# Kernel tuning notes

Measured on AMD Instinct MI355X. Metric: run time of the kernel, lower is better.

Reference implementation:

```python
import jax, jax.numpy as jnp
import numpy as np

B, C, IC, H, W = 16, 256, 128, 32, 32  # batch, in_channels, inter_channels, spatial
EPS = 1e-5


def _conv1x1(x, w, b=None):
    # x: [B,C,H,W], w: [O,C] -> [B,O,H,W]
    y = jnp.einsum('bchw,oc->bohw', x, w)
    if b is not None:
        y = y + b[None, :, None, None]
    return y


def _dot_kernel(x, wt, wp):
    # relu-matmul attention, symmetrized, degree-rsqrt normalized with zero masking
    b, _, h, w = x.shape
    n = h * w
    t = jnp.maximum(_conv1x1(x, wt), 0.0).reshape(b, -1, n)  # [B,IC,N]
    p = jnp.maximum(_conv1x1(x, wp), 0.0).reshape(b, -1, n)  # [B,IC,N]
    att = jnp.einsum('bcn,bcm->bnm', t, p)                    # [B,N,N]
    att = (att + att.transpose(0, 2, 1)) * 0.5
    d = att.sum(axis=2)                                       # [B,N]
    dinv = jnp.where(d != 0, jax.lax.rsqrt(jnp.where(d != 0, d, 1.0)), 0.0)
    return att * dinv[:, None, :] * dinv[:, :, None]


def _bn(x, gamma, beta):
    # BatchNorm2d in training mode (batch statistics, biased variance)
    mu = jnp.mean(x, axis=(0, 2, 3), keepdims=True)
    var = jnp.mean((x - mu) ** 2, axis=(0, 2, 3), keepdims=True)
    xhat = (x - mu) * jax.lax.rsqrt(var + EPS)
    return xhat * gamma[None, :, None, None] + beta[None, :, None, None]


def setup_inputs() -> dict:
    key = jax.random.key(0)
    ks = jax.random.split(key, 32)
    s = 0.05
    inp = {
        'x':  jax.random.normal(ks[0], (B, C, H, W), jnp.float32),
        'ob': jax.random.normal(ks[1], (B, C, H, W), jnp.float32),
        'od': jax.random.normal(ks[2], (B, C, H, W), jnp.float32),
        'Wt': jax.random.normal(ks[3], (IC, C), jnp.float32) * s,
        'Wp': jax.random.normal(ks[4], (IC, C), jnp.float32) * s,
        'Wgx': jax.random.normal(ks[5], (IC, C), jnp.float32) * s,
        'bgx': jax.random.normal(ks[6], (IC,), jnp.float32) * s,
        'Wgb': jax.random.normal(ks[7], (IC, C), jnp.float32) * s,
        'bgb': jax.random.normal(ks[8], (IC,), jnp.float32) * s,
        'Wgd': jax.random.normal(ks[9], (IC, C), jnp.float32) * s,
        'bgd': jax.random.normal(ks[10], (IC,), jnp.float32) * s,
        'Wwx': jax.random.normal(ks[11], (C, IC), jnp.float32) * s,
        'bwx': jax.random.normal(ks[12], (C,), jnp.float32) * s,
        'Wwb': jax.random.normal(ks[13], (C, IC), jnp.float32) * s,
        'bwb': jax.random.normal(ks[14], (C,), jnp.float32) * s,
        'Wwd': jax.random.normal(ks[15], (C, IC), jnp.float32) * s,
        'bwd': jax.random.normal(ks[16], (C,), jnp.float32) * s,
        'Wwxb': jax.random.normal(ks[17], (C, IC), jnp.float32) * s,
        'bwxb': jax.random.normal(ks[18], (C,), jnp.float32) * s,
        'Wwxd': jax.random.normal(ks[19], (C, IC), jnp.float32) * s,
        'bwxd': jax.random.normal(ks[20], (C,), jnp.float32) * s,
        'gamma1': jnp.ones((C,), jnp.float32),
        'beta1': jnp.zeros((C,), jnp.float32),
        'gamma2': jnp.ones((C,), jnp.float32),
        'beta2': jnp.zeros((C,), jnp.float32),
        'Wout': jax.random.normal(ks[21], (C, C), jnp.float32) * s,
        'bout': jax.random.normal(ks[22], (C,), jnp.float32) * s,
    }
    return inp


def reference(x, ob, od, Wt, Wp, Wgx, bgx, Wgb, bgb, Wgd, bgd,
              Wwx, bwx, Wwb, bwb, Wwd, bwd, Wwxb, bwxb, Wwxd, bwxd,
              gamma1, beta1, gamma2, beta2, Wout, bout):
    b, c, h, w = x.shape
    n = h * w

    def g_tokens(inp, wg, bg):
        return _conv1x1(inp, wg, bg).reshape(b, -1, n).transpose(0, 2, 1)  # [B,N,IC]

    g_x = g_tokens(x, Wgx, bgx)
    g_b = g_tokens(ob, Wgb, bgb)
    g_d = g_tokens(od, Wgd, bgd)

    f_x = _dot_kernel(x, Wt, Wp)
    f_b = _dot_kernel(ob, Wt, Wp)
    f_d = _dot_kernel(od, Wt, Wp)

    def agg(f, g):
        # bmm(f,g).transpose(1,2).view(B,IC,H,W)
        return jnp.einsum('bnm,bmi->bin', f, g).reshape(b, -1, h, w)

    x_self = _conv1x1(agg(f_x, g_x), Wwx, bwx)
    ob_self = _conv1x1(agg(f_b, g_b), Wwb, bwb)
    od_self = _conv1x1(agg(f_d, g_d), Wwd, bwd)
    x_ob_cross = _conv1x1(agg(f_b, g_x), Wwxb, bwxb)
    x_od_cross = _conv1x1(agg(f_d, g_x), Wwxd, bwxd)

    od_final = _bn(od_self + x_ob_cross, gamma1, beta1)
    ob_final = _bn(ob_self + x_od_cross, gamma2, beta2)
    output = _conv1x1(od_final + ob_final + x_self, Wout, bout)
    return output + x
```

## Files before the change

kernel.cpp:

```cpp
#include <hip/hip_runtime.h>

#define GAS __attribute__((address_space(1)))
#define LAS __attribute__((address_space(3)))

typedef __attribute__((ext_vector_type(8))) short short8;
typedef __attribute__((ext_vector_type(4))) float f32x4;
typedef unsigned short u16;

constexpr int cB = 16, cC = 256, cIC = 128, cN = 1024;

__device__ __forceinline__ u16 f2bf(float v) {
    unsigned u = __builtin_bit_cast(unsigned, v);
    return (u16)((u + 0x7fffu + ((u >> 16) & 1u)) >> 16);
}
__device__ __forceinline__ float bf2f(u16 v) {
    unsigned u = ((unsigned)v) << 16;
    return __builtin_bit_cast(float, u);
}
__device__ __forceinline__ float rsz(float d) {
    return (d != 0.0f) ? rsqrtf(d) : 0.0f;
}

template<int N> __device__ __forceinline__ void wait_vmcnt() {
    if constexpr (N == 0) asm volatile("s_waitcnt vmcnt(0)" ::: "memory");
    else if constexpr (N == 1) asm volatile("s_waitcnt vmcnt(1)" ::: "memory");
    else if constexpr (N == 2) asm volatile("s_waitcnt vmcnt(2)" ::: "memory");
    else if constexpr (N == 3) asm volatile("s_waitcnt vmcnt(3)" ::: "memory");
    else if constexpr (N == 4) asm volatile("s_waitcnt vmcnt(4)" ::: "memory");
    else if constexpr (N == 5) asm volatile("s_waitcnt vmcnt(5)" ::: "memory");
    else if constexpr (N == 6) asm volatile("s_waitcnt vmcnt(6)" ::: "memory");
}

template<int BM, int BN, int WR, int WC, bool BREMAP = false>
__device__ __forceinline__ void gemm_core(
    const u16* __restrict__ Ab, const u16* __restrict__ Ab2, int ksplit, int lda,
    const u16* __restrict__ Bb, int ldb, int K,
    u16* lsA, u16* lsB,
    f32x4 (&acc)[BM/(WR*16)][BN/(WC*16)])
{
    constexpr int THREADS = WR * WC * 64;
    constexpr int MR = BM / (WR * 16), NR = BN / (WC * 16);
    constexpr int ACH = (BM * 64) / (THREADS * 16);
    constexpr int BCH = (BN * 64) / (THREADS * 16);
    constexpr int RPC = THREADS / 4;
    constexpr int ISSUES = ACH + BCH;

    const int tid  = threadIdx.x;
    const int lane = tid & 63;
    const int wave = tid >> 6;
    const int wr = wave / WC, wc = wave % WC;
    const int r0 = tid >> 2, slot = tid & 3;

    auto stage = [&](int buf, int kk) {
        const u16* Ak = (Ab2 != nullptr && kk >= ksplit) ? (Ab2 + (kk - ksplit)) : (Ab + kk);
        const u16* Bk = Bb + (BREMAP ? (((kk >> 7) << 8) + (kk & 127)) : kk);
        #pragma unroll
        for (int c = 0; c < ACH; c++) {
            int row = c * RPC + r0;
            int sk = (slot ^ ((row >> 1) & 3)) << 3;
            __builtin_amdgcn_global_load_lds((GAS void*)(Ak + (size_t)row * lda + sk),
                (LAS void*)(lsA + buf * (BM * 32) + c * (THREADS * 8) + (wave << 9)), 16, 0, 0);
        }
        #pragma unroll
        for (int c = 0; c < BCH; c++) {
            int row = c * RPC + r0;
            int sk = (slot ^ ((row >> 1) & 3)) << 3;
            __builtin_amdgcn_global_load_lds((GAS void*)(Bk + (size_t)row * ldb + sk),
                (LAS void*)(lsB + buf * (BN * 32) + c * (THREADS * 8) + (wave << 9)), 16, 0, 0);
        }
    };

    stage(0, 0);
    const int nt = K >> 5;
    for (int t = 0; t < nt; t++) {
        const int cur = t & 1;
        if (t + 1 < nt) { stage(cur ^ 1, (t + 1) << 5); wait_vmcnt<ISSUES>(); }
        else            wait_vmcnt<0>();
        __builtin_amdgcn_s_barrier();
        asm volatile("" ::: "memory");

        const u16* la = lsA + cur * (BM * 32);
        const u16* lb = lsB + cur * (BN * 32);
        short8 af[MR], bf[NR];
        #pragma unroll
        for (int m = 0; m < MR; m++) {
            int row = wr * (BM / WR) + (m << 4) + (lane & 15);
            af[m] = *(const short8*)&la[(row << 5) + (((lane >> 4) ^ ((row >> 1) & 3)) << 3)];
        }
        #pragma unroll
        for (int n = 0; n < NR; n++) {
            int row = wc * (BN / WC) + (n << 4) + (lane & 15);
            bf[n] = *(const short8*)&lb[(row << 5) + (((lane >> 4) ^ ((row >> 1) & 3)) << 3)];
        }
        #pragma unroll
        for (int m = 0; m < MR; m++)
            #pragma unroll
            for (int n = 0; n < NR; n++)
                acc[m][n] = __builtin_amdgcn_mfma_f32_16x16x32_bf16(af[m], bf[n], acc[m][n], 0, 0, 0);

        asm volatile("s_waitcnt lgkmcnt(0)" ::: "memory");
        __builtin_amdgcn_sched_barrier(0);
        __builtin_amdgcn_s_barrier();
    }
}

template<int BM, int BN, int WR, int WC, bool RELU, bool OBF16, bool RBIAS, bool RESID>
__global__ __launch_bounds__(WR*WC*64) void gemm_bt(
    const u16* __restrict__ A, long long sA, long long sA2, int lda,
    const u16* __restrict__ B, long long sB, long long sB2, int ldb,
    void* __restrict__ C, long long sC, long long sC2, int ldc,
    int K,
    const float* __restrict__ bias, int sb2,
    const float* __restrict__ resid, long long sR)
{
    __shared__ alignas(16) u16 lsA[2 * BM * 32];
    __shared__ alignas(16) u16 lsB[2 * BN * 32];

    const int lane = threadIdx.x & 63;
    const int wave = threadIdx.x >> 6;
    const int wr = wave / WC, wc = wave % WC;
    const int zlo = blockIdx.z & 15, zhi = blockIdx.z >> 4;

    const u16* Ab = A + zlo * sA + zhi * sA2 + (size_t)(blockIdx.x * BM) * lda;
    const u16* Bb = B + zlo * sB + zhi * sB2 + (size_t)(blockIdx.y * BN) * ldb;

    f32x4 acc[BM/(WR*16)][BN/(WC*16)] = {};
    gemm_core<BM, BN, WR, WC>(Ab, nullptr, K, lda, Bb, ldb, K, lsA, lsB, acc);

    const int rowb = blockIdx.x * BM + wr * (BM / WR) + ((lane >> 4) << 2);
    const int colb = blockIdx.y * BN + wc * (BN / WC) + (lane & 15);
    const long long cbase = zlo * sC + zhi * sC2;
    #pragma unroll
    for (int m = 0; m < BM/(WR*16); m++) {
        #pragma unroll
        for (int n = 0; n < BN/(WC*16); n++) {
            #pragma unroll
            for (int r = 0; r < 4; r++) {
                int row = rowb + m * 16 + r;
                int col = colb + n * 16;
                float v = acc[m][n][r];
                if (RBIAS) v += bias[zhi * sb2 + row];
                if (RESID) v += resid[zlo * sR + (size_t)row * ldc + col];
                if (RELU)  v = fmaxf(v, 0.0f);
                if (OBF16) ((u16*)C)[cbase + (size_t)row * ldc + col] = f2bf(v);
                else       ((float*)C)[cbase + (size_t)row * ldc + col] = v;
            }
        }
    }
}

__global__ __launch_bounds__(512) void tp_gemm(
    const u16* __restrict__ XT, const u16* __restrict__ WTP,
    u16* __restrict__ TPt, u16* __restrict__ TP, float* __restrict__ CS)
{
    __shared__ alignas(16) u16 lsA[2 * 128 * 32];
    __shared__ alignas(16) u16 lsB[2 * 256 * 32];

    const int id = blockIdx.x;
    const int lane = threadIdx.x & 63;
    const int wave = threadIdx.x >> 6;
    const int wr = wave >> 2, wc = wave & 3;

    if (id < 384) {
        const int z = id >> 3, r_ = id & 7, cx = r_ >> 2, ny = r_ & 3;
        const u16* Ab = WTP + (size_t)(cx * 128) * 256;
        const u16* Bb = XT + (size_t)z * 262144 + (size_t)(ny * 256) * 256;
        f32x4 acc[4][4] = {};
        gemm_core<128, 256, 2, 4>(Ab, nullptr, 256, 256, Bb, 256, 256, lsA, lsB, acc);

        const int rowb = cx * 128 + wr * 64 + ((lane >> 4) << 2);
        const int colb = ny * 256 + wc * 64 + (lane & 15);
        u16* Cb = TPt + (size_t)z * 262144;
        float rp[4][4] = {};
        #pragma unroll
        for (int m = 0; m < 4; m++)
            #pragma unroll
            for (int n = 0; n < 4; n++)
                #pragma unroll
                for (int r = 0; r < 4; r++) {
                    float v = fmaxf(acc[m][n][r], 0.0f);
                    Cb[(size_t)(rowb + m * 16 + r) * 1024 + colb + n * 16] = f2bf(v);
                    rp[m][r] += v;
                }
        #pragma unroll
        for (int m = 0; m < 4; m++)
            #pragma unroll
            for (int r = 0; r < 4; r++) {
                float v = rp[m][r];
                v += __shfl_xor(v, 1, 64);
                v += __shfl_xor(v, 2, 64);
                v += __shfl_xor(v, 4, 64);
                v += __shfl_xor(v, 8, 64);
                if ((lane & 15) == 0)
                    atomicAdd(&CS[z * 256 + rowb + m * 16 + r], v);
            }
    } else {
        const int id2 = id - 384;
        const int z = id2 >> 3, nx = id2 & 7;
        const u16* Ab = XT + (size_t)z * 262144 + (size_t)(nx * 128) * 256;
        f32x4 acc[4][4] = {};
        gemm_core<128, 256, 2, 4>(Ab, nullptr, 256, 256, WTP, 256, 256, lsA, lsB, acc);

        const int rowb = nx * 128 + wr * 64 + ((lane >> 4) << 2);
        const int colb = wc * 64 + (lane & 15);
        u16* Cb = TP + (size_t)z * 262144;
        #pragma unroll
        for (int m = 0; m < 4; m++)
            #pragma unroll
            for (int n = 0; n < 4; n++)
                #pragma unroll
                for (int r = 0; r < 4; r++)
                    Cb[(size_t)(rowb + m * 16 + r) * 256 + colb + n * 16] =
                        f2bf(fmaxf(acc[m][n][r], 0.0f));
    }
}

__global__ __launch_bounds__(256) void dinv_mv(
    const u16* __restrict__ TPt, const float* __restrict__ CS, float* __restrict__ DINV)
{
    const int z = blockIdx.y;
    const int n = blockIdx.x * 256 + threadIdx.x;
    __shared__ float ws[256];
    ws[threadIdx.x] = 0.5f * CS[z * 256 + (threadIdx.x ^ 128)];
    __syncthreads();
    const u16* base = TPt + (size_t)z * 262144 + n;
    float d = 0;
    #pragma unroll 8
    for (int c = 0; c < 256; c++) d += bf2f(base[(size_t)c << 10]) * ws[c];
    DINV[(z << 10) + n] = d;
}

__global__ __launch_bounds__(256) void g_gemm(
    const u16* __restrict__ XT, const u16* __restrict__ WG,
    const float* __restrict__ BG, const float* __restrict__ DINV,
    u16* __restrict__ GXp, u16* __restrict__ GBp, u16* __restrict__ GDp)
{
    __shared__ alignas(16) u16 lsA[2 * 128 * 32];
    __shared__ alignas(16) u16 lsB[2 * 128 * 32];

    const int yb = blockIdx.x, zs = blockIdx.z;
    const int stream = zs >> 4, b = zs & 15;

    const u16* Ab = WG + stream * 32768;
    const u16* Bb = XT + (size_t)zs * 262144 + (size_t)(yb * 128) * 256;

    f32x4 acc[4][4] = {};
    gemm_core<128, 128, 2, 2>(Ab, nullptr, 256, 256, Bb, 256, 256, lsA, lsB, acc);

    const int lane = threadIdx.x & 63;
    const int wave = threadIdx.x >> 6;
    const int wr = wave >> 1, wc = wave & 1;
    const int rowb = (wr << 6) + ((lane >> 4) << 2);
    const int colb = yb * 128 + (wc << 6) + (lane & 15);
    const float* dvx = DINV + (b << 10);
    const float* dvb = DINV + 16384 + (b << 10);
    const float* dvd = DINV + 32768 + (b << 10);
    float sx[4], sb_[4], sd[4];
    #pragma unroll
    for (int n = 0; n < 4; n++) {
        int col = colb + n * 16;
        if (stream == 0) { sx[n] = rsz(dvx[col]); sb_[n] = rsz(dvb[col]); sd[n] = rsz(dvd[col]); }
        else if (stream == 1) sb_[n] = rsz(dvb[col]);
        else sd[n] = rsz(dvd[col]);
    }
    #pragma unroll
    for (int m = 0; m < 4; m++) {
        #pragma unroll
        for (int r = 0; r < 4; r++) {
            int row = rowb + m * 16 + r;
            float bias = BG[stream * 128 + row];
            #pragma unroll
            for (int n = 0; n < 4; n++) {
                int col = colb + n * 16;
                float v = acc[m][n][r] + bias;
                if (stream == 0) {
                    GXp[(size_t)b * 131072 + ((size_t)row << 10) + col] = f2bf(v * sx[n]);
                    GBp[(size_t)b * 262144 + ((size_t)(row + 128) << 10) + col] = f2bf(v * sb_[n]);
                    GDp[(size_t)b * 262144 + ((size_t)(row + 128) << 10) + col] = f2bf(v * sd[n]);
                } else if (stream == 1) {
                    GBp[(size_t)b * 262144 + ((size_t)row << 10) + col] = f2bf(v * sb_[n]);
                } else {
                    GDp[(size_t)b * 262144 + ((size_t)row << 10) + col] = f2bf(v * sd[n]);
                }
            }
        }
    }
}

__global__ __launch_bounds__(256) void inner_splitk(
    const u16* __restrict__ TPt, const u16* __restrict__ GXp,
    const u16* __restrict__ GBp, const u16* __restrict__ GDp,
    u16* __restrict__ MX, u16* __restrict__ MB, u16* __restrict__ MD)
{
    __shared__ alignas(16) u16 lsA[2 * 128 * 32];
    __shared__ alignas(16) u16 lsB[2 * 128 * 32];

    const int bz = blockIdx.z;
    const int split = bz / 48, z = bz % 48;
    const int which = z >> 4, b = z & 15;
    if (which == 0 && blockIdx.y) return;
    const u16* Gp = (which == 0) ? GXp : (which == 1) ? GBp : GDp;
    u16* M = (which == 0) ? MX : (which == 1) ? MB : MD;
    const int JD  = (which == 0) ? 128 : 256;
    const int ldc = 2 * JD;
    const long long sB = (which == 0) ? 131072 : 262144;

    const u16* Ab = TPt + (size_t)z * 262144 + (size_t)(blockIdx.x * 128) * 1024 + split * 512;
    const u16* Bb = Gp + (size_t)b * sB + (size_t)(blockIdx.y * 128) * 1024 + split * 512;

    f32x4 acc[4][4] = {};
    gemm_core<128, 128, 2, 2>(Ab, nullptr, 512, 1024, Bb, 1024, 512, lsA, lsB, acc);

    const int lane = threadIdx.x & 63;
    const int wave = threadIdx.x >> 6;
    const int wr = wave >> 1, wc = wave & 1;
    const int rowb = blockIdx.x * 128 + (wr << 6) + ((lane >> 4) << 2);
    const int colb = blockIdx.y * 128 + (wc << 6) + (lane & 15);
    u16* Cb = M + (size_t)b * (256 * ldc);
    #pragma unroll
    for (int m = 0; m < 4; m++)
        #pragma unroll
        for (int n = 0; n < 4; n++)
            #pragma unroll
            for (int r = 0; r < 4; r++) {
                int row = (rowb + m * 16 + r) ^ 128;
                int col = split * JD + colb + n * 16;
                Cb[(size_t)row * ldc + col] = f2bf(acc[m][n][r]);
            }
}

__global__ __launch_bounds__(512) void fold_gemm(
    const u16* __restrict__ WF2, const u16* __restrict__ MX,
    const u16* __restrict__ MB, const u16* __restrict__ MD,
    u16* __restrict__ FF2)
{
    __shared__ alignas(16) u16 lsA[2 * 128 * 32];
    __shared__ alignas(16) u16 lsB[2 * 256 * 32];

    const int z = blockIdx.z, q = z >> 4, b = z & 15;
    const int pr = (q == 4) ? 2 : (q >> 1);
    const int side = (q == 1 || q == 3) ? 1 : 0;

    const u16* Ab = WF2 + q * 65536 + (size_t)(blockIdx.x * 128) * 256;

    f32x4 acc[4][4] = {};
    if (q == 4) {
        const u16* Bb = MX + (size_t)b * 65536;
        gemm_core<128, 256, 2, 4, false>(Ab, nullptr, 256, 256, Bb, 256, 256, lsA, lsB, acc);
    } else {
        const u16* Mp = (q == 1 || q == 2) ? MB : MD;
        const int coff = side ? 128 : 0;
        const u16* Bb = Mp + (size_t)b * 131072 + coff;
        gemm_core<128, 256, 2, 4, true>(Ab, nullptr, 256, 256, Bb, 512, 256, lsA, lsB, acc);
    }

    const int lane = threadIdx.x & 63;
    const int wave = threadIdx.x >> 6;
    const int wr = wave >> 2, wc = wave & 3;
    const int rowb = blockIdx.x * 128 + wr * 64 + ((lane >> 4) << 2);
    const int colb = wc * 64 + (lane & 15);
    u16* Cb = FF2 + (size_t)pr * 2097152 + (size_t)b * 131072;
    #pragma unroll
    for (int m = 0; m < 4; m++)
        #pragma unroll
        for (int n = 0; n < 4; n++)
            #pragma unroll
            for (int r = 0; r < 4; r++)
                Cb[(size_t)(rowb + m * 16 + r) * 512 + side * 256 + colb + n * 16]
                    = f2bf(acc[m][n][r]);
}

__global__ __launch_bounds__(512) void outer_gemm(
    const u16* __restrict__ TP, const u16* __restrict__ FF2,
    const float* __restrict__ DINV,
    u16* __restrict__ SALL, float* __restrict__ BNA)
{
    __shared__ alignas(16) u16 lsA[2 * 128 * 32];
    __shared__ alignas(16) u16 lsB[2 * 256 * 32];

    const int z = blockIdx.z, zhi = z >> 4, b = z & 15;
    const int sa1[3] = {2, 1, 0}, sa2[3] = {1, 2, 0};

    const int lane = threadIdx.x & 63;
    const int wave = threadIdx.x >> 6;
    const int wr = wave >> 2, wc = wave & 3;
    const int rowb = blockIdx.x * 128 + wr * 64 + ((lane >> 4) << 2);
    const int colb = wc * 64 + (lane & 15);

    const u16* A1 = TP + (size_t)(sa1[zhi] * 16 + b) * 262144 + (size_t)(blockIdx.x * 128) * 256;
    const u16* B1 = FF2 + (size_t)zhi * 2097152 + (size_t)b * 131072;
    const float* dv1 = DINV + sa1[zhi] * 16384 + (b << 10);

    f32x4 acc[4][4] = {};
    gemm_core<128, 256, 2, 4>(A1, nullptr, 256, 256, B1, 512, 256, lsA, lsB, acc);

    f32x4 keep[4][4];
    #pragma unroll
    for (int m = 0; m < 4; m++) {
        f32x4 dva;
        #pragma unroll
        for (int r = 0; r < 4; r++) dva[r] = rsz(dv1[rowb + m * 16 + r]);
        #pragma unroll
        for (int n = 0; n < 4; n++) keep[m][n] = acc[m][n] * dva;
    }

    if (zhi < 2) {
        const u16* A2 = TP + (size_t)(sa2[zhi] * 16 + b) * 262144 + (size_t)(blockIdx.x * 128) * 256;
        const u16* B2 = B1 + 256;
        const float* dv2 = DINV + sa2[zhi] * 16384 + (b << 10);
        #pragma unroll
        for (int m = 0; m < 4; m++)
            #pragma unroll
            for (int n = 0; n < 4; n++) acc[m][n] = f32x4{0.f, 0.f, 0.f, 0.f};
        gemm_core<128, 256, 2, 4>(A2, nullptr, 256, 256, B2, 512, 256, lsA, lsB, acc);
        #pragma unroll
        for (int m = 0; m < 4; m++) {
            f32x4 dva;
            #pragma unroll
            for (int r = 0; r < 4; r++) dva[r] = rsz(dv2[rowb + m * 16 + r]);
            #pragma unroll
            for (int n = 0; n < 4; n++) keep[m][n] = keep[m][n] + acc[m][n] * dva;
        }
    }

    u16* Cb = SALL + (size_t)b * 786432;
    float csum[4] = {}, csq[4] = {};
    #pragma unroll
    for (int m = 0; m < 4; m++)
        #pragma unroll
        for (int n = 0; n < 4; n++)
            #pragma unroll
            for (int r = 0; r < 4; r++) {
                float v = keep[m][n][r];
                Cb[(size_t)(rowb + m * 16 + r) * 768 + zhi * 256 + colb + n * 16] = f2bf(v);
                csum[n] += v;
                csq[n] += v * v;
            }
    if (zhi < 2) {
        #pragma unroll
        for (int n = 0; n < 4; n++) {
            float s = csum[n], q = csq[n];
            s += __shfl_xor(s, 16, 64); s += __shfl_xor(s, 32, 64);
            q += __shfl_xor(q, 16, 64); q += __shfl_xor(q, 32, 64);
            if (lane < 16) {
                atomicAdd(&BNA[zhi * 512 + colb + n * 16], s);
                atomicAdd(&BNA[zhi * 512 + 256 + colb + n * 16], q);
            }
        }
    }
}

__global__ __launch_bounds__(256) void bnscale(
    const float* __restrict__ Wout, const float* __restrict__ g1, const float* __restrict__ be1,
    const float* __restrict__ g2, const float* __restrict__ be2,
    const float* __restrict__ bwx, const float* __restrict__ bout,
    const float* __restrict__ BNA, u16* __restrict__ WoutS, float* __restrict__ BIAS2)
{
    int o = blockIdx.x, c = threadIdx.x;
    const float inv = 1.0f / 16384.0f;
    float m1 = BNA[c] * inv;
    float v1 = BNA[256 + c] * inv - m1 * m1;
    float sc1 = g1[c] * rsqrtf(v1 + 1e-5f), sh1 = be1[c] - m1 * sc1;
    float m2 = BNA[512 + c] * inv;
    float v2 = BNA[768 + c] * inv - m2 * m2;
    float sc2 = g2[c] * rsqrtf(v2 + 1e-5f), sh2 = be2[c] - m2 * sc2;
    float wv = Wout[o * 256 + c];
    WoutS[o * 768 + c]       = f2bf(wv * sc1);
    WoutS[o * 768 + 256 + c] = f2bf(wv * sc2);
    WoutS[o * 768 + 512 + c] = f2bf(wv);
    __shared__ float red[256];
    red[c] = wv * (sh1 + sh2 + bwx[c]);
    __syncthreads();
    for (int s = 128; s; s >>= 1) { if (c < s) red[c] += red[c + s]; __syncthreads(); }
    if (c == 0) BIAS2[o] = red[0] + bout[o];
}

__global__ void prep_transpose(const float* __restrict__ x, const float* __restrict__ ob,
                               const float* __restrict__ od, u16* __restrict__ xt,
                               const float* Wt, const float* Wp,
                               const float* Wgx, const float* Wgb, const float* Wgd,
                               const float* bgx, const float* bgb, const float* bgd,
                               const float* Wwd, const float* Wwxb, const float* Wwb,
                               const float* Wwxd, const float* Wwx,
                               u16* wtp, u16* wg, u16* wf2, float* bg,
                               float* __restrict__ ZZ)
{
    int tx = threadIdx.x, ty = threadIdx.y;
    if (blockIdx.z == 48) {
        int t = (blockIdx.y * 32 + blockIdx.x) * 256 + ty * 32 + tx;
        wtp[t] = f2bf(t < 32768 ? Wt[t] : Wp[t - 32768]);
        if (t < 32768) {
            wg[t] = f2bf(Wgx[t]); wg[32768 + t] = f2bf(Wgb[t]); wg[65536 + t] = f2bf(Wgd[t]);
        }
        {
            int o = t >> 8, k = t & 255, j = k & 127;
            const float* Wq[5] = {Wwd, Wwxb, Wwb, Wwxd, Wwx};
            #pragma unroll
            for (int q = 0; q < 5; q++)
                wf2[q * 65536 + t] = f2bf(0.5f * Wq[q][o * 128 + j]);
        }
        if (t < 384) bg[t] = (t < 128) ? bgx[t] : (t < 256) ? bgb[t - 128] : bgd[t - 256];
        if (t < 13312) ZZ[t] = 0.0f;
        return;
    }
    __shared__ float tbuf[32][33];
    int z = blockIdx.z, which = z >> 4, b = z & 15;
    const float* src = (which == 0) ? x : (which == 1) ? ob : od;
    const float* s = src + (size_t)b * cC * cN;
    u16* dst = xt + (size_t)which * (cB * cN * cC) + (size_t)b * (cN * cC);
    int n0 = blockIdx.x << 5, c0 = blockIdx.y << 5;
    #pragma unroll
    for (int i = 0; i < 4; i++) { int r = ty + (i << 3); tbuf[r][tx] = s[(size_t)(c0 + r) * cN + n0 + tx]; }
    __syncthreads();
    #pragma unroll
    for (int i = 0; i < 4; i++) { int r = ty + (i << 3); dst[(size_t)(n0 + r) * cC + c0 + tx] = f2bf(tbuf[tx][r]); }
}

extern "C" void kernel_launch(void* const* d_in, const int* in_sizes, int n_in,
                              void* d_out, int out_size, void* d_ws, size_t ws_size,
                              hipStream_t stream)
{
    const float* x    = (const float*)d_in[0];
    const float* ob   = (const float*)d_in[1];
    const float* od   = (const float*)d_in[2];
    const float* Wt   = (const float*)d_in[3];
    const float* Wp   = (const float*)d_in[4];
    const float* Wgx  = (const float*)d_in[5];
    const float* bgx  = (const float*)d_in[6];
    const float* Wgb  = (const float*)d_in[7];
    const float* bgb  = (const float*)d_in[8];
    const float* Wgd  = (const float*)d_in[9];
    const float* bgd  = (const float*)d_in[10];
    const float* Wwx  = (const float*)d_in[11];
    const float* bwx  = (const float*)d_in[12];
    const float* Wwb  = (const float*)d_in[13];
    const float* Wwd  = (const float*)d_in[15];
    const float* Wwxb = (const float*)d_in[17];
    const float* Wwxd = (const float*)d_in[19];
    const float* g1   = (const float*)d_in[21];
    const float* be1  = (const float*)d_in[22];
    const float* g2   = (const float*)d_in[23];
    const float* be2  = (const float*)d_in[24];
    const float* Wout = (const float*)d_in[25];
    const float* bout = (const float*)d_in[26];
    float* out = (float*)d_out;

    char* w = (char*)d_ws;
    u16*   XT    = (u16*)(w);
    u16*   TPt   = (u16*)(w + 25165824);
    u16*   TP    = (u16*)(w + 50331648);
    u16*   GXp   = (u16*)(w + 75497472);
    u16*   GBp   = (u16*)(w + 79691776);
    u16*   GDp   = (u16*)(w + 88080384);
    u16*   MX    = (u16*)(w + 96468992);
    u16*   MB    = (u16*)(w + 98566144);
    u16*   MD    = (u16*)(w + 102760448);
    u16*   FF2   = (u16*)(w + 106954752);
    u16*   WTP   = (u16*)(w + 119537664);
    u16*   WG    = (u16*)(w + 119668736);
    u16*   WF2   = (u16*)(w + 119865344);
    u16*   WoutS = (u16*)(w + 120520704);
    float* BGf   = (float*)(w + 120913920);
    float* BIAS2 = (float*)(w + 120915968);
    float* DINV  = (float*)(w + 120920064);
    float* ZZ    = (float*)(w + 121116672);

    float* CS   = ZZ;
    float* BNA  = ZZ + 12288;
    u16*   SALL = TPt;

    prep_transpose<<<dim3(32, 8, 49), dim3(32, 8), 0, stream>>>(
        x, ob, od, XT, Wt, Wp, Wgx, Wgb, Wgd, bgx, bgb, bgd,
        Wwd, Wwxb, Wwb, Wwxd, Wwx, WTP, WG, WF2, BGf, ZZ);

    tp_gemm<<<dim3(768), 512, 0, stream>>>(XT, WTP, TPt, TP, CS);

    dinv_mv<<<dim3(4, 48), 256, 0, stream>>>(TPt, CS, DINV);

    g_gemm<<<dim3(8, 1, 48), 256, 0, stream>>>(XT, WG, BGf, DINV, GXp, GBp, GDp);

    inner_splitk<<<dim3(2, 2, 96), 256, 0, stream>>>(TPt, GXp, GBp, GDp, MX, MB, MD);

    fold_gemm<<<dim3(2, 1, 80), 512, 0, stream>>>(WF2, MX, MB, MD, FF2);

    outer_gemm<<<dim3(8, 1, 48), 512, 0, stream>>>(TP, FF2, DINV, SALL, BNA);

    bnscale<<<dim3(256), 256, 0, stream>>>(Wout, g1, be1, g2, be2, bwx, bout,
                                           BNA, WoutS, BIAS2);

    gemm_bt<128, 128, 2, 2, false, false, true, true><<<dim3(2, 8, 16), 256, 0, stream>>>(
        WoutS, 0, 0, 768,  SALL, 786432, 0, 768,  out, 262144, 0, 1024,
        768, BIAS2, 0, x, 262144);
}
```

Before: 167.3 us.

## Fuse degree matvec into g_gemm and vectorize prep transpose with 64x64 tiles

Removes the separate dinv_mv kernel. Each g_gemm block now computes the degree values for its own 128 columns, for every stream it needs, before its GEMM and keeps the rsqrt results in shared memory. Stream-0 blocks redo the b and d stream matvecs, so some work is duplicated, but one launch and a round trip through global memory go away. The prep transpose moves to 64x64 tiles with float4 loads and short8 bf16 stores. The weight-conversion branch loops four times per thread to match the new grid. A spare vmcnt(8) wait case is also added.

```diff
diff --git a/kernel.cpp b/kernel.cpp
--- a/kernel.cpp
+++ b/kernel.cpp
@@ -29,6 +29,7 @@
     else if constexpr (N == 4) asm volatile("s_waitcnt vmcnt(4)" ::: "memory");
     else if constexpr (N == 5) asm volatile("s_waitcnt vmcnt(5)" ::: "memory");
     else if constexpr (N == 6) asm volatile("s_waitcnt vmcnt(6)" ::: "memory");
+    else if constexpr (N == 8) asm volatile("s_waitcnt vmcnt(8)" ::: "memory");
 }
 
 template<int BM, int BN, int WR, int WC, bool BREMAP = false>
@@ -215,31 +216,44 @@
     }
 }
 
-__global__ __launch_bounds__(256) void dinv_mv(
-    const u16* __restrict__ TPt, const float* __restrict__ CS, float* __restrict__ DINV)
-{
-    const int z = blockIdx.y;
-    const int n = blockIdx.x * 256 + threadIdx.x;
-    __shared__ float ws[256];
-    ws[threadIdx.x] = 0.5f * CS[z * 256 + (threadIdx.x ^ 128)];
-    __syncthreads();
-    const u16* base = TPt + (size_t)z * 262144 + n;
-    float d = 0;
-    #pragma unroll 8
-    for (int c = 0; c < 256; c++) d += bf2f(base[(size_t)c << 10]) * ws[c];
-    DINV[(z << 10) + n] = d;
-}
-
 __global__ __launch_bounds__(256) void g_gemm(
     const u16* __restrict__ XT, const u16* __restrict__ WG,
-    const float* __restrict__ BG, const float* __restrict__ DINV,
+    const float* __restrict__ BG, const u16* __restrict__ TPt,
+    const float* __restrict__ CS, float* __restrict__ DINV,
     u16* __restrict__ GXp, u16* __restrict__ GBp, u16* __restrict__ GDp)
 {
     __shared__ alignas(16) u16 lsA[2 * 128 * 32];
     __shared__ alignas(16) u16 lsB[2 * 128 * 32];
+    __shared__ float ws[256];
+    __shared__ float part[2][128];
+    __shared__ float dvs[3][128];
 
     const int yb = blockIdx.x, zs = blockIdx.z;
     const int stream = zs >> 4, b = zs & 15;
+    const int tid = threadIdx.x;
+
+    const int nstr = (stream == 0) ? 3 : 1;
+    for (int si = 0; si < nstr; si++) {
+        const int s = (stream == 0) ? si : stream;
+        const int z2 = s * 16 + b;
+        ws[tid] = 0.5f * CS[z2 * 256 + (tid ^ 128)];
+        __syncthreads();
+        const int col = tid & 127, half = tid >> 7;
+        const u16* base = TPt + (size_t)z2 * 262144 + (size_t)(half * 128) * 1024
+                        + yb * 128 + col;
+        float a = 0;
+        #pragma unroll 8
+        for (int c = 0; c < 128; c++)
+            a += bf2f(base[(size_t)c << 10]) * ws[half * 128 + c];
+        part[half][col] = a;
+        __syncthreads();
+        if (tid < 128) {
+            float d = part[0][tid] + part[1][tid];
+            if (s == stream) DINV[(zs << 10) + yb * 128 + tid] = d;
+            dvs[si][tid] = rsz(d);
+        }
+        __syncthreads();
+    }
 
     const u16* Ab = WG + stream * 32768;
     const u16* Bb = XT + (size_t)zs * 262144 + (size_t)(yb * 128) * 256;
@@ -251,17 +265,15 @@
     const int wave = threadIdx.x >> 6;
     const int wr = wave >> 1, wc = wave & 1;
     const int rowb = (wr << 6) + ((lane >> 4) << 2);
-    const int colb = yb * 128 + (wc << 6) + (lane & 15);
-    const float* dvx = DINV + (b << 10);
-    const float* dvb = DINV + 16384 + (b << 10);
-    const float* dvd = DINV + 32768 + (b << 10);
+    const int lcolb = (wc << 6) + (lane & 15);
+    const int colb = yb * 128 + lcolb;
     float sx[4], sb_[4], sd[4];
     #pragma unroll
     for (int n = 0; n < 4; n++) {
-        int col = colb + n * 16;
-        if (stream == 0) { sx[n] = rsz(dvx[col]); sb_[n] = rsz(dvb[col]); sd[n] = rsz(dvd[col]); }
-        else if (stream == 1) sb_[n] = rsz(dvb[col]);
-        else sd[n] = rsz(dvd[col]);
+        int lc = lcolb + n * 16;
+        if (stream == 0) { sx[n] = dvs[0][lc]; sb_[n] = dvs[1][lc]; sd[n] = dvs[2][lc]; }
+        else if (stream == 1) sb_[n] = dvs[0][lc];
+        else sd[n] = dvs[0][lc];
     }
     #pragma unroll
     for (int m = 0; m < 4; m++) {
@@ -475,45 +487,63 @@
     if (c == 0) BIAS2[o] = red[0] + bout[o];
 }
 
-__global__ void prep_transpose(const float* __restrict__ x, const float* __restrict__ ob,
-                               const float* __restrict__ od, u16* __restrict__ xt,
-                               const float* Wt, const float* Wp,
-                               const float* Wgx, const float* Wgb, const float* Wgd,
-                               const float* bgx, const float* bgb, const float* bgd,
-                               const float* Wwd, const float* Wwxb, const float* Wwb,
-                               const float* Wwxd, const float* Wwx,
-                               u16* wtp, u16* wg, u16* wf2, float* bg,
-                               float* __restrict__ ZZ)
-{
-    int tx = threadIdx.x, ty = threadIdx.y;
+__global__ __launch_bounds__(256) void prep_transpose(
+    const float* __restrict__ x, const float* __restrict__ ob,
+    const float* __restrict__ od, u16* __restrict__ xt,
+    const float* Wt, const float* Wp,
+    const float* Wgx, const float* Wgb, const float* Wgd,
+    const float* bgx, const float* bgb, const float* bgd,
+    const float* Wwd, const float* Wwxb, const float* Wwb,
+    const float* Wwxd, const float* Wwx,
+    u16* wtp, u16* wg, u16* wf2, float* bg,
+    float* __restrict__ ZZ)
+{
+    const int tid = threadIdx.x;
     if (blockIdx.z == 48) {
-        int t = (blockIdx.y * 32 + blockIdx.x) * 256 + ty * 32 + tx;
-        wtp[t] = f2bf(t < 32768 ? Wt[t] : Wp[t - 32768]);
-        if (t < 32768) {
-            wg[t] = f2bf(Wgx[t]); wg[32768 + t] = f2bf(Wgb[t]); wg[65536 + t] = f2bf(Wgd[t]);
-        }
-        {
-            int o = t >> 8, k = t & 255, j = k & 127;
-            const float* Wq[5] = {Wwd, Wwxb, Wwb, Wwxd, Wwx};
-            #pragma unroll
-            for (int q = 0; q < 5; q++)
-                wf2[q * 65536 + t] = f2bf(0.5f * Wq[q][o * 128 + j]);
-        }
-        if (t < 384) bg[t] = (t < 128) ? bgx[t] : (t < 256) ? bgb[t - 128] : bgd[t - 256];
-        if (t < 13312) ZZ[t] = 0.0f;
+        int base = (blockIdx.y * 16 + blockIdx.x) * 1024;
+        #pragma unroll
+        for (int l = 0; l < 4; l++) {
+            int t = base + l * 256 + tid;
+            wtp[t] = f2bf(t < 32768 ? Wt[t] : Wp[t - 32768]);
+            if (t < 32768) {
+                wg[t] = f2bf(Wgx[t]); wg[32768 + t] = f2bf(Wgb[t]); wg[65536 + t] = f2bf(Wgd[t]);
+            }
+            {
+                int o = t >> 8, k = t & 255, j = k & 127;
+                const float* Wq[5] = {Wwd, Wwxb, Wwb, Wwxd, Wwx};
+                #pragma unroll
+                for (int q = 0; q < 5; q++)
+                    wf2[q * 65536 + t] = f2bf(0.5f * Wq[q][o * 128 + j]);
+            }
+            if (t < 384) bg[t] = (t < 128) ? bgx[t] : (t < 256) ? bgb[t - 128] : bgd[t - 256];
+            if (t < 13312) ZZ[t] = 0.0f;
+        }
         return;
     }
-    __shared__ float tbuf[32][33];
-    int z = blockIdx.z, which = z >> 4, b = z & 15;
+    __shared__ float ls[64][68];
+    const int z = blockIdx.z, which = z >> 4, b = z & 15;
     const float* src = (which == 0) ? x : (which == 1) ? ob : od;
     const float* s = src + (size_t)b * cC * cN;
-    u16* dst = xt + (size_t)which * (cB * cN * cC) + (size_t)b * (cN * cC);
-    int n0 = blockIdx.x << 5, c0 = blockIdx.y << 5;
-    #pragma unroll
-    for (int i = 0; i < 4; i++) { int r = ty + (i << 3); tbuf[r][tx] = s[(size_t)(c0 + r) * cN + n0 + tx]; }
+    u16* dst = xt + (size_t)z * (cN * cC);
+    const int n0 = blockIdx.x << 6, c0 = blockIdx.y << 6;
+
+    const int cl0 = tid >> 4, n4 = (tid & 15) << 2;
+    #pragma unroll
+    for (int p = 0; p < 4; p++) {
+        int cl = cl0 + (p << 4);
+        f32x4 v = *(const f32x4*)&s[(size_t)(c0 + cl) * cN + n0 + n4];
+        ls[cl][n4] = v[0]; ls[cl][n4 + 1] = v[1]; ls[cl][n4 + 2] = v[2]; ls[cl][n4 + 3] = v[3];
+    }
     __syncthreads();
-    #pragma unroll
-    for (int i = 0; i < 4; i++) { int r = ty + (i << 3); dst[(size_t)(n0 + r) * cC + c0 + tx] = f2bf(tbuf[tx][r]); }
+    const int nl0 = tid >> 3, c8 = (tid & 7) << 3;
+    #pragma unroll
+    for (int q = 0; q < 2; q++) {
+        int nl = nl0 + (q << 5);
+        short8 o;
+        #pragma unroll
+        for (int j = 0; j < 8; j++) o[j] = (short)f2bf(ls[c8 + j][nl]);
+        *(short8*)&dst[(size_t)(n0 + nl) * 256 + c0 + c8] = o;
+    }
 }
 
 extern "C" void kernel_launch(void* const* d_in, const int* in_sizes, int n_in,
@@ -569,15 +599,14 @@
     float* BNA  = ZZ + 12288;
     u16*   SALL = TPt;
 
-    prep_transpose<<<dim3(32, 8, 49), dim3(32, 8), 0, stream>>>(
+    prep_transpose<<<dim3(16, 4, 49), 256, 0, stream>>>(
         x, ob, od, XT, Wt, Wp, Wgx, Wgb, Wgd, bgx, bgb, bgd,
         Wwd, Wwxb, Wwb, Wwxd, Wwx, WTP, WG, WF2, BGf, ZZ);
 
     tp_gemm<<<dim3(768), 512, 0, stream>>>(XT, WTP, TPt, TP, CS);
 
-    dinv_mv<<<dim3(4, 48), 256, 0, stream>>>(TPt, CS, DINV);
-
-    g_gemm<<<dim3(8, 1, 48), 256, 0, stream>>>(XT, WG, BGf, DINV, GXp, GBp, GDp);
+    g_gemm<<<dim3(8, 1, 48), 256, 0, stream>>>(XT, WG, BGf, TPt, CS, DINV,
+                                               GXp, GBp, GDp);
 
     inner_splitk<<<dim3(2, 2, 96), 256, 0, stream>>>(TPt, GXp, GBp, GDp, MX, MB, MD);
 
```

Measured after the change: 170.6 us. 1.02x slower.
